# Kernel tuning notes

Measured on AMD Instinct MI355X. Metric: run time of the kernel, lower is better.

## Reference

```python
import jax, jax.numpy as jnp
import numpy as np

WIN = 7            # skimage default win_size
K1 = 0.01
K2 = 0.03
DATA_RANGE = 1.0   # images are in [0, 1]
PAD = (WIN - 1) // 2


def _uniform_filter_valid(x):
    # x: [N, 1, H, W] -> valid 7x7 box filter (== skimage uniform_filter cropped by PAD)
    k = jnp.ones((1, 1, WIN, WIN), x.dtype) / (WIN * WIN)
    return jax.lax.conv_general_dilated(
        x, k, window_strides=(1, 1), padding='VALID',
        dimension_numbers=('NCHW', 'OIHW', 'NCHW'))


def _ssim_mean(a, b):
    # a, b: [B, C, H, W]; each [H, W] slice is one independent SSIM image
    B, C, H, W = a.shape
    x = a.reshape(B * C, 1, H, W)
    y = b.reshape(B * C, 1, H, W)

    ux = _uniform_filter_valid(x)
    uy = _uniform_filter_valid(y)
    uxx = _uniform_filter_valid(x * x)
    uyy = _uniform_filter_valid(y * y)
    uxy = _uniform_filter_valid(x * y)

    NP = WIN * WIN
    cov_norm = NP / (NP - 1.0)  # sample covariance correction (skimage default)
    vx = cov_norm * (uxx - ux * ux)
    vy = cov_norm * (uyy - uy * uy)
    vxy = cov_norm * (uxy - ux * uy)

    C1 = (K1 * DATA_RANGE) ** 2
    C2 = (K2 * DATA_RANGE) ** 2

    S = ((2.0 * ux * uy + C1) * (2.0 * vxy + C2)) / \
        ((ux * ux + uy * uy + C1) * (vx + vy + C2))

    # skimage crops PAD border then means; VALID conv already cropped it.
    # All images are the same size, so np.average(per-image means) == global mean.
    return jnp.mean(S)


def setup_inputs() -> dict:
    key = jax.random.key(0)
    k1, k2 = jax.random.split(key)
    pred = jax.random.uniform(k1, (32, 4, 384, 384), dtype=jnp.float32)
    actual = jax.random.uniform(k2, (32, 4, 384, 384), dtype=jnp.float32)
    return {"pred": pred, "actual": actual}


def reference(pred, actual):
    return _ssim_mean(pred, actual)
```

## Files before the change

### kernel.cpp

```cpp
#include <hip/hip_runtime.h>

#define WIN 7
#define OUT_W 126
#define OUT_H 15
#define IN_W 132
#define IN_H 21
#define PITCH 132
#define AELEM (OUT_H * PITCH)
#define H 384
#define W 384
#define OH 378
#define OW 378
#define NIMG 128
#define TX 3
#define TY 26
#define NBLK (TX * TY * NIMG)

__device__ __forceinline__ float wave_reduce(float v) {
#pragma unroll
    for (int off = 32; off > 0; off >>= 1) v += __shfl_down(v, off, 64);
    return v;
}

__global__ __launch_bounds__(256, 4) void ssim_main(const float* __restrict__ pred,
                                                    const float* __restrict__ act,
                                                    float* __restrict__ partials) {
    __shared__ __align__(16) float cs[5 * AELEM + 16];
    __shared__ float red[4];

    const int t = threadIdx.x;
    const int img = blockIdx.z;
    const int x0 = blockIdx.x * OUT_W;
    const int y0 = blockIdx.y * OUT_H;
    const size_t base = (size_t)img * H * W;

    if (t < IN_W) {
        const int col = x0 + t;
        const float* xc = pred + base + col;
        const float* yc = act + base + col;
        float xv[IN_H], yv[IN_H];
#pragma unroll
        for (int i = 0; i < IN_H; ++i) {
            const int row = y0 + i;
            const bool ok = row < H;
            xv[i] = ok ? xc[(size_t)row * W] : 0.f;
            yv[i] = ok ? yc[(size_t)row * W] : 0.f;
        }
        float sx = 0.f, sy = 0.f, sxx = 0.f, syy = 0.f, sxy = 0.f;
#pragma unroll
        for (int k = 0; k < WIN; ++k) {
            sx += xv[k];
            sy += yv[k];
            sxx = fmaf(xv[k], xv[k], sxx);
            syy = fmaf(yv[k], yv[k], syy);
            sxy = fmaf(xv[k], yv[k], sxy);
        }
        cs[0 * AELEM + t] = sx;
        cs[1 * AELEM + t] = sy;
        cs[2 * AELEM + t] = sxx;
        cs[3 * AELEM + t] = syy;
        cs[4 * AELEM + t] = sxy;
#pragma unroll
        for (int r = 1; r < OUT_H; ++r) {
            const float xn = xv[r + 6], yn = yv[r + 6];
            const float xo = xv[r - 1], yo = yv[r - 1];
            sx += xn - xo;
            sy += yn - yo;
            sxx = fmaf(xn, xn, fmaf(-xo, xo, sxx));
            syy = fmaf(yn, yn, fmaf(-yo, yo, syy));
            sxy = fmaf(xn, yn, fmaf(-xo, yo, sxy));
            const int a = r * PITCH + t;
            cs[0 * AELEM + a] = sx;
            cs[1 * AELEM + a] = sy;
            cs[2 * AELEM + a] = sxx;
            cs[3 * AELEM + a] = syy;
            cs[4 * AELEM + a] = sxy;
        }
    }
    __syncthreads();

    const int r = t & 15;
    const int g = t >> 4;
    const int c0 = g * 8;

    const float C1B = 0.2401f;
    const float C2B = 2.1168f;

    float acc = 0.f;
    if (r < OUT_H && (y0 + r) < OH) {
        float S[5][8];
#pragma unroll
        for (int a = 0; a < 5; ++a) {
            const float* bp = &cs[a * AELEM + r * PITCH + c0];
            const float4 q0 = *(const float4*)(bp);
            const float4 q1 = *(const float4*)(bp + 4);
            const float4 q2 = *(const float4*)(bp + 8);
            const float4 q3 = *(const float4*)(bp + 12);
            const float v[16] = {q0.x, q0.y, q0.z, q0.w, q1.x, q1.y, q1.z, q1.w,
                                 q2.x, q2.y, q2.z, q2.w, q3.x, q3.y, q3.z, q3.w};
            float s = ((v[0] + v[1]) + (v[2] + v[3])) + ((v[4] + v[5]) + v[6]);
            S[a][0] = s;
#pragma unroll
            for (int j = 1; j < 8; ++j) {
                s += v[j + 6] - v[j - 1];
                S[a][j] = s;
            }
        }
        const int nmax = OUT_W - c0;
#pragma unroll
        for (int j = 0; j < 8; ++j) {
            if (j < nmax) {
                const float Sx = S[0][j], Sy = S[1][j];
                const float Sxx = S[2][j], Syy = S[3][j], Sxy = S[4][j];
                const float p = Sx * Sy;
                const float q = fmaf(Sx, Sx, Sy * Sy);
                const float n1 = fmaf(2.f, p, C1B);
                const float n2 = fmaf(98.f, Sxy, fmaf(-2.f, p, C2B));
                const float d1 = q + C1B;
                const float d2 = fmaf(49.f, Sxx + Syy, C2B - q);
                acc = fmaf(n1 * n2, __builtin_amdgcn_rcpf(d1 * d2), acc);
            }
        }
    }

    const float wsum = wave_reduce(acc);
    if ((t & 63) == 0) red[t >> 6] = wsum;
    __syncthreads();
    if (t == 0) {
        partials[blockIdx.x + TX * (blockIdx.y + TY * blockIdx.z)] =
            red[0] + red[1] + red[2] + red[3];
    }
}

__global__ __launch_bounds__(1024) void ssim_finalize(const float* __restrict__ partials,
                                                      float* __restrict__ out) {
    __shared__ double red[1024];
    const int t = threadIdx.x;
    double s = 0.0;
    for (int i = t; i < NBLK; i += 1024) s += (double)partials[i];
    red[t] = s;
    __syncthreads();
#pragma unroll
    for (int off = 512; off > 0; off >>= 1) {
        if (t < off) red[t] += red[t + off];
        __syncthreads();
    }
    if (t == 0) out[0] = (float)(red[0] / ((double)NIMG * OH * OW));
}

extern "C" void kernel_launch(void* const* d_in, const int* in_sizes, int n_in,
                              void* d_out, int out_size, void* d_ws, size_t ws_size,
                              hipStream_t stream) {
    const float* pred = (const float*)d_in[0];
    const float* act  = (const float*)d_in[1];
    float* partials = (float*)d_ws;
    dim3 grid(TX, TY, NIMG);
    ssim_main<<<grid, 256, 0, stream>>>(pred, act, partials);
    ssim_finalize<<<1, 1024, 0, stream>>>(partials, (float*)d_out);
}
```

Baseline: 170.0 us.

## Merge squared sums and interleave column sums as float4 in shared memory

Sums x*x and y*y into one accumulator, since only their sum is used, cutting the per-pixel quantities from five to four. The column sums are stored as an interleaved float4 per column in shared memory rather than five separate planes. The output tile height becomes 16 so every thread in the block does horizontal work. Each thread then loads 14 float4 values and runs a sliding-window sum. This reduces shared-memory traffic, arithmetic and idle threads, at the cost of a padded pitch and some wasted loads past the valid columns.

```diff
diff --git a/kernel.cpp b/kernel.cpp
--- a/kernel.cpp
+++ b/kernel.cpp
@@ -2,18 +2,17 @@
 
 #define WIN 7
 #define OUT_W 126
-#define OUT_H 15
+#define OUT_H 16
 #define IN_W 132
-#define IN_H 21
-#define PITCH 132
-#define AELEM (OUT_H * PITCH)
+#define IN_H 22
+#define APITCH 532
 #define H 384
 #define W 384
 #define OH 378
 #define OW 378
 #define NIMG 128
 #define TX 3
-#define TY 26
+#define TY 24
 #define NBLK (TX * TY * NIMG)
 
 __device__ __forceinline__ float wave_reduce(float v) {
@@ -25,14 +24,13 @@
 __global__ __launch_bounds__(256, 4) void ssim_main(const float* __restrict__ pred,
                                                     const float* __restrict__ act,
                                                     float* __restrict__ partials) {
-    __shared__ __align__(16) float cs[5 * AELEM + 16];
+    __shared__ __align__(16) float A[OUT_H * APITCH + 4];
     __shared__ float red[4];
 
     const int t = threadIdx.x;
-    const int img = blockIdx.z;
     const int x0 = blockIdx.x * OUT_W;
     const int y0 = blockIdx.y * OUT_H;
-    const size_t base = (size_t)img * H * W;
+    const size_t base = (size_t)blockIdx.z * H * W;
 
     if (t < IN_W) {
         const int col = x0 + t;
@@ -46,35 +44,25 @@
             xv[i] = ok ? xc[(size_t)row * W] : 0.f;
             yv[i] = ok ? yc[(size_t)row * W] : 0.f;
         }
-        float sx = 0.f, sy = 0.f, sxx = 0.f, syy = 0.f, sxy = 0.f;
+        float sx = 0.f, sy = 0.f, sq = 0.f, sxy = 0.f;
 #pragma unroll
         for (int k = 0; k < WIN; ++k) {
             sx += xv[k];
             sy += yv[k];
-            sxx = fmaf(xv[k], xv[k], sxx);
-            syy = fmaf(yv[k], yv[k], syy);
+            sq = fmaf(xv[k], xv[k], fmaf(yv[k], yv[k], sq));
             sxy = fmaf(xv[k], yv[k], sxy);
         }
-        cs[0 * AELEM + t] = sx;
-        cs[1 * AELEM + t] = sy;
-        cs[2 * AELEM + t] = sxx;
-        cs[3 * AELEM + t] = syy;
-        cs[4 * AELEM + t] = sxy;
+        float* ap = &A[t * 4];
+        *(float4*)ap = make_float4(sx, sy, sq, sxy);
 #pragma unroll
         for (int r = 1; r < OUT_H; ++r) {
             const float xn = xv[r + 6], yn = yv[r + 6];
             const float xo = xv[r - 1], yo = yv[r - 1];
             sx += xn - xo;
             sy += yn - yo;
-            sxx = fmaf(xn, xn, fmaf(-xo, xo, sxx));
-            syy = fmaf(yn, yn, fmaf(-yo, yo, syy));
+            sq = fmaf(xn, xn, fmaf(yn, yn, fmaf(-xo, xo, fmaf(-yo, yo, sq))));
             sxy = fmaf(xn, yn, fmaf(-xo, yo, sxy));
-            const int a = r * PITCH + t;
-            cs[0 * AELEM + a] = sx;
-            cs[1 * AELEM + a] = sy;
-            cs[2 * AELEM + a] = sxx;
-            cs[3 * AELEM + a] = syy;
-            cs[4 * AELEM + a] = sxy;
+            *(float4*)(ap + r * APITCH) = make_float4(sx, sy, sq, sxy);
         }
     }
     __syncthreads();
@@ -86,40 +74,32 @@
     const float C1B = 0.2401f;
     const float C2B = 2.1168f;
 
+    const float4* qp = (const float4*)&A[r * APITCH + c0 * 4];
+    float4 q[14];
+#pragma unroll
+    for (int k = 0; k < 14; ++k) q[k] = qp[k];
+
     float acc = 0.f;
-    if (r < OUT_H && (y0 + r) < OH) {
-        float S[5][8];
+    if (y0 + r < OH) {
+        float Sx = 0.f, Sy = 0.f, Sq = 0.f, Sxy = 0.f;
 #pragma unroll
-        for (int a = 0; a < 5; ++a) {
-            const float* bp = &cs[a * AELEM + r * PITCH + c0];
-            const float4 q0 = *(const float4*)(bp);
-            const float4 q1 = *(const float4*)(bp + 4);
-            const float4 q2 = *(const float4*)(bp + 8);
-            const float4 q3 = *(const float4*)(bp + 12);
-            const float v[16] = {q0.x, q0.y, q0.z, q0.w, q1.x, q1.y, q1.z, q1.w,
-                                 q2.x, q2.y, q2.z, q2.w, q3.x, q3.y, q3.z, q3.w};
-            float s = ((v[0] + v[1]) + (v[2] + v[3])) + ((v[4] + v[5]) + v[6]);
-            S[a][0] = s;
-#pragma unroll
-            for (int j = 1; j < 8; ++j) {
-                s += v[j + 6] - v[j - 1];
-                S[a][j] = s;
-            }
+        for (int k = 0; k < WIN - 1; ++k) {
+            Sx += q[k].x; Sy += q[k].y; Sq += q[k].z; Sxy += q[k].w;
         }
-        const int nmax = OUT_W - c0;
 #pragma unroll
         for (int j = 0; j < 8; ++j) {
-            if (j < nmax) {
-                const float Sx = S[0][j], Sy = S[1][j];
-                const float Sxx = S[2][j], Syy = S[3][j], Sxy = S[4][j];
-                const float p = Sx * Sy;
-                const float q = fmaf(Sx, Sx, Sy * Sy);
-                const float n1 = fmaf(2.f, p, C1B);
-                const float n2 = fmaf(98.f, Sxy, fmaf(-2.f, p, C2B));
-                const float d1 = q + C1B;
-                const float d2 = fmaf(49.f, Sxx + Syy, C2B - q);
-                acc = fmaf(n1 * n2, __builtin_amdgcn_rcpf(d1 * d2), acc);
-            }
+            Sx += q[j + 6].x; Sy += q[j + 6].y; Sq += q[j + 6].z; Sxy += q[j + 6].w;
+
+            const float p = Sx * Sy;
+            const float qq = fmaf(Sx, Sx, Sy * Sy);
+            const float n1 = fmaf(2.f, p, C1B);
+            const float n2 = fmaf(98.f, Sxy, fmaf(-2.f, p, C2B));
+            const float d1 = qq + C1B;
+            const float d2 = fmaf(49.f, Sq, C2B - qq);
+            const float s = (n1 * n2) * __builtin_amdgcn_rcpf(d1 * d2);
+            acc = (c0 + j < OUT_W) ? acc + s : acc;
+
+            Sx -= q[j].x; Sy -= q[j].y; Sq -= q[j].z; Sxy -= q[j].w;
         }
     }
 
```

Measured after the change: 174.4 us. 1.03x slower.
